# Optimization experiments

Hardware: AMD Instinct MI355X
Metric: run time of the kernel (lower is better)

The kernel has to match this reference:

```python
import jax, jax.numpy as jnp
import numpy as np

N_NODES = 100000
N_EDGES = 3200000
IN_DIM, BIG, HID = 4, 32, 2
EPS = 1e-5


def _lin_init(key, fan_in, fan_out):
    # torch nn.Linear default: U(-1/sqrt(fan_in), 1/sqrt(fan_in))
    kw, kb = jax.random.split(key)
    bound = 1.0 / np.sqrt(fan_in)
    w = jax.random.uniform(kw, (fan_in, fan_out), minval=-bound, maxval=bound, dtype=jnp.float32)
    b = jax.random.uniform(kb, (fan_out,), minval=-bound, maxval=bound, dtype=jnp.float32)
    return w, b


def setup_inputs() -> dict:
    key = jax.random.key(0)
    ks = jax.random.split(key, 9)
    x = jax.random.normal(ks[0], (N_NODES, IN_DIM), dtype=jnp.float32)
    edge_index = jax.random.randint(ks[1], (2, N_EDGES), 0, N_NODES, dtype=jnp.int32)
    bn_w = jnp.ones((IN_DIM,), jnp.float32)
    bn_b = jnp.zeros((IN_DIM,), jnp.float32)
    enc_w1, enc_b1 = _lin_init(ks[2], 2 * IN_DIM, BIG)
    enc_w2, enc_b2 = _lin_init(ks[3], BIG, BIG)
    enc_w3, enc_b3 = _lin_init(ks[4], BIG, HID)
    dec_w1, dec_b1 = _lin_init(ks[5], 2 * HID, BIG)
    dec_w2, dec_b2 = _lin_init(ks[6], BIG, BIG)
    dec_w3, dec_b3 = _lin_init(ks[7], BIG, IN_DIM)
    return dict(x=x, edge_index=edge_index, bn_w=bn_w, bn_b=bn_b,
                enc_w1=enc_w1, enc_b1=enc_b1, enc_w2=enc_w2, enc_b2=enc_b2,
                enc_w3=enc_w3, enc_b3=enc_b3,
                dec_w1=dec_w1, dec_b1=dec_b1, dec_w2=dec_w2, dec_b2=dec_b2,
                dec_w3=dec_w3, dec_b3=dec_b3)


def _edge_conv(x, src, dst, w1, b1, w2, b2, w3, b3, final_relu):
    # PyG EdgeConv: message = nn(cat([x_i, x_j - x_i])), mean-aggregated at target i (=dst)
    xi = x[dst]                     # [E, F] gather (target)
    xj = x[src]                     # [E, F] gather (source)
    h = jnp.concatenate([xi, xj - xi], axis=-1)  # [E, 2F]
    h = jax.nn.relu(h @ w1 + b1)
    h = jax.nn.relu(h @ w2 + b2)
    h = h @ w3 + b3
    if final_relu:
        h = jax.nn.relu(h)
    n = x.shape[0]
    agg = jax.ops.segment_sum(h, dst, num_segments=n)          # [N, out]
    cnt = jax.ops.segment_sum(jnp.ones((h.shape[0],), h.dtype), dst, num_segments=n)
    return agg / jnp.maximum(cnt, 1.0)[:, None]


def reference(x, edge_index, bn_w, bn_b,
              enc_w1, enc_b1, enc_w2, enc_b2, enc_w3, enc_b3,
              dec_w1, dec_b1, dec_w2, dec_b2, dec_w3, dec_b3):
    # BatchNorm1d (training mode: batch statistics, biased variance)
    mu = jnp.mean(x, axis=0)
    var = jnp.var(x, axis=0)
    h = (x - mu) * jax.lax.rsqrt(var + EPS) * bn_w + bn_b
    src, dst = edge_index[0], edge_index[1]
    h = _edge_conv(h, src, dst, enc_w1, enc_b1, enc_w2, enc_b2, enc_w3, enc_b3, final_relu=True)
    h = _edge_conv(h, src, dst, dec_w1, dec_b1, dec_w2, dec_b2, dec_w3, dec_b3, final_relu=False)
    return h
```

## Files before the change

### kernel.cpp

```cpp
#include <hip/hip_runtime.h>

#define N_NODES 100000
#define N_EDGES 3200000
#define EPS 1e-5f
#define NODE_BLOCKS 391
#define NB 782
#define BSTRIDE 4608
#define NSUB 9
#define S1_EPB 8192
#define S1_BLOCKS 391

typedef unsigned int uint;
typedef uint u32x4 __attribute__((ext_vector_type(4)));
typedef _Float16 f16x8 __attribute__((ext_vector_type(8)));
typedef float f32x16 __attribute__((ext_vector_type(16)));

static __device__ __forceinline__ f16x8 as_h8(u32x4 u) { return __builtin_bit_cast(f16x8, u); }
static __device__ __forceinline__ uint pkh(float a, float b) {
    return __builtin_bit_cast(uint, __builtin_amdgcn_cvt_pkrtz(a, b));
}
static __device__ __forceinline__ void swap32(uint& a, uint& b) {
    asm volatile("v_permlane32_swap_b32 %0, %1" : "+v"(a), "+v"(b));
}

#define OFF_STATS  0
#define OFF_BCNT   1024
#define OFF_INVCNT 5120
#define OFF_AGG1   405120
#define OFF_DECW   1205120
#define OFF_BUCKET 1214848
#define OFF_PENC   15629696
#define OFF_PCNT   22836608
#define OFF_PDEC   26440064
#define OFF_ENCW   26440064

__global__ __launch_bounds__(256) void k_bn_stats(const float* __restrict__ x,
                                                  double* __restrict__ stats) {
    int i = blockIdx.x * 256 + threadIdx.x;
    float4 v = make_float4(0.f, 0.f, 0.f, 0.f);
    if (i < N_NODES) v = ((const float4*)x)[i];
    double a[8];
    a[0] = v.x; a[1] = v.y; a[2] = v.z; a[3] = v.w;
    a[4] = (double)v.x * v.x; a[5] = (double)v.y * v.y;
    a[6] = (double)v.z * v.z; a[7] = (double)v.w * v.w;
    #pragma unroll
    for (int off = 32; off > 0; off >>= 1) {
        #pragma unroll
        for (int j = 0; j < 8; j++) a[j] += __shfl_down(a[j], off);
    }
    __shared__ double smem[4][8];
    int wave = threadIdx.x >> 6;
    int lane = threadIdx.x & 63;
    if (lane == 0) {
        #pragma unroll
        for (int j = 0; j < 8; j++) smem[wave][j] = a[j];
    }
    __syncthreads();
    if (threadIdx.x == 0) {
        #pragma unroll
        for (int j = 0; j < 8; j++) {
            double t = smem[0][j] + smem[1][j] + smem[2][j] + smem[3][j];
            atomicAdd(&stats[j], t);
        }
    }
}

static __device__ __forceinline__ void packhl(float v0, float v1, uint* ph, uint* pl) {
    _Float16 h0 = (_Float16)v0, h1 = (_Float16)v1;
    float r0 = v0 - (float)h0, r1 = v1 - (float)h1;
    _Float16 l0 = (_Float16)r0, l1 = (_Float16)r1;
    *ph = (uint)__builtin_bit_cast(unsigned short, h0) |
          ((uint)__builtin_bit_cast(unsigned short, h1) << 16);
    *pl = (uint)__builtin_bit_cast(unsigned short, l0) |
          ((uint)__builtin_bit_cast(unsigned short, l1) << 16);
}

__global__ __launch_bounds__(256) void k_prep(const float* __restrict__ ew1,
                                              const float* __restrict__ eb1,
                                              const float* __restrict__ ew2,
                                              const float* __restrict__ dw1,
                                              const float* __restrict__ db1,
                                              const float* __restrict__ dw2,
                                              uint* __restrict__ encw,
                                              uint* __restrict__ decw) {
    int t = threadIdx.x;
    int lane = t >> 2, d = t & 3, hi = lane >> 5, m = lane & 31;
    int k0 = 8 * hi + 2 * d;
    uint h, l;
    {
        float v0 = (k0 < 8) ? ew1[k0 * 32 + m] : (k0 == 8 ? eb1[m] : 0.f);
        float v1 = (k0 + 1 < 8) ? ew1[(k0 + 1) * 32 + m] : 0.f;
        packhl(v0, v1, &h, &l);
        encw[t] = h; encw[256 + t] = l;
    }
    #pragma unroll
    for (int kt = 0; kt < 2; kt++) {
        int k = 16 * kt + k0;
        packhl(ew2[k * 32 + m], ew2[(k + 1) * 32 + m], &h, &l);
        encw[512 + kt * 256 + t] = h; encw[1024 + kt * 256 + t] = l;
    }
    {
        float v0 = (k0 < 4) ? dw1[k0 * 32 + m] : (k0 == 4 ? db1[m] : 0.f);
        float v1 = (k0 + 1 < 4) ? dw1[(k0 + 1) * 32 + m] : 0.f;
        packhl(v0, v1, &h, &l);
        decw[t] = h; decw[256 + t] = l;
    }
    #pragma unroll
    for (int kt = 0; kt < 2; kt++) {
        int k = 16 * kt + k0;
        packhl(dw2[k * 32 + m], dw2[(k + 1) * 32 + m], &h, &l);
        decw[512 + kt * 256 + t] = h; decw[1024 + kt * 256 + t] = l;
    }
}

__global__ __launch_bounds__(256) void k_s1(const int* __restrict__ ei,
                                            int* __restrict__ bcnt,
                                            int* __restrict__ bucket_buf) {
    __shared__ int hist[NB];
    __shared__ int base[NB];
    __shared__ int run[NB];
    __shared__ int gbase[NB];
    __shared__ int entries[S1_EPB];
    __shared__ unsigned short bk16[S1_EPB];
    __shared__ int wsum[4];
    int tid = threadIdx.x;
    int e0 = blockIdx.x * S1_EPB;
    for (int i = tid; i < NB; i += 256) hist[i] = 0;
    __syncthreads();
    #pragma unroll
    for (int k = 0; k < 32; k++) {
        int e = e0 + k * 256 + tid;
        if (e < N_EDGES) atomicAdd(&hist[ei[N_EDGES + e] >> 7], 1);
    }
    __syncthreads();
    int t4 = tid * 4;
    int h0 = (t4 + 0 < NB) ? hist[t4 + 0] : 0;
    int h1 = (t4 + 1 < NB) ? hist[t4 + 1] : 0;
    int h2 = (t4 + 2 < NB) ? hist[t4 + 2] : 0;
    int h3 = (t4 + 3 < NB) ? hist[t4 + 3] : 0;
    int tsum = h0 + h1 + h2 + h3;
    int lane = tid & 63, wv = tid >> 6;
    int xs = tsum;
    #pragma unroll
    for (int off = 1; off < 64; off <<= 1) {
        int u = __shfl_up(xs, off);
        if (lane >= off) xs += u;
    }
    if (lane == 63) wsum[wv] = xs;
    __syncthreads();
    int wo = 0;
    #pragma unroll
    for (int w = 0; w < 4; w++) if (w < wv) wo += wsum[w];
    int texcl = wo + xs - tsum;
    if (t4 + 0 < NB) base[t4 + 0] = texcl;
    if (t4 + 1 < NB) base[t4 + 1] = texcl + h0;
    if (t4 + 2 < NB) base[t4 + 2] = texcl + h0 + h1;
    if (t4 + 3 < NB) base[t4 + 3] = texcl + h0 + h1 + h2;
    __syncthreads();
    for (int i = tid; i < NB; i += 256) {
        int h = hist[i];
        gbase[i] = i * BSTRIDE + (h ? atomicAdd(&bcnt[i], h) : 0);
        run[i] = base[i];
    }
    __syncthreads();
    #pragma unroll
    for (int k = 0; k < 32; k++) {
        int e = e0 + k * 256 + tid;
        if (e < N_EDGES) {
            int s = ei[e];
            int d = ei[N_EDGES + e];
            int b = d >> 7;
            int r = atomicAdd(&run[b], 1);
            entries[r] = s | ((d & 127) << 17);
            bk16[r] = (unsigned short)b;
        }
    }
    __syncthreads();
    int nloc = min(S1_EPB, N_EDGES - e0);
    for (int idx = tid; idx < nloc; idx += 256) {
        int b = bk16[idx];
        bucket_buf[gbase[b] + (idx - base[b])] = entries[idx];
    }
}

__global__ __launch_bounds__(256, 3) void k_enc_partial(const float* __restrict__ x,
                                                        const double* __restrict__ stats,
                                                        const float* __restrict__ bn_w,
                                                        const float* __restrict__ bn_b,
                                                        const int* __restrict__ bucket_buf,
                                                        const int* __restrict__ bcnt,
                                                        float2* __restrict__ penc,
                                                        int* __restrict__ pcnt,
                                                        const uint* __restrict__ encw,
                                                        const float* __restrict__ b2,
                                                        const float* __restrict__ w3,
                                                        const float* __restrict__ b3) {
    __shared__ float4 xhat[128];
    __shared__ float acc0[128], acc1[128];
    __shared__ int lc[128];
    __shared__ __align__(8) float w3s[64];
    int b = blockIdx.x, sub = blockIdx.y, tid = threadIdx.x;
    int lane = tid & 63, hi = lane >> 5, col = lane & 31, wv = tid >> 6;
    int cb = bcnt[b];
    int node0 = b << 7;

    const double inv_n = 1.0 / (double)N_NODES;
    float sc[4], sh[4];
    #pragma unroll
    for (int d = 0; d < 4; d++) {
        double m  = stats[d] * inv_n;
        double vr = stats[4 + d] * inv_n - m * m;
        float rs  = (float)(1.0 / sqrt(vr + (double)EPS));
        sc[d] = rs * bn_w[d];
        sh[d] = bn_b[d] - (float)m * sc[d];
    }

    if (tid < 128) {
        acc0[tid] = 0.f; acc1[tid] = 0.f; lc[tid] = 0;
        int n = node0 + tid;
        if (n < N_NODES) {
            float4 v = ((const float4*)x)[n];
            xhat[tid] = make_float4(fmaf(v.x, sc[0], sh[0]), fmaf(v.y, sc[1], sh[1]),
                                    fmaf(v.z, sc[2], sh[2]), fmaf(v.w, sc[3], sh[3]));
        }
    }
    if (tid < 64) w3s[tid] = w3[tid];
    __syncthreads();

    const u32x4* e4 = (const u32x4*)encw;
    u32x4 w1h = e4[lane],        w1l = e4[64 + lane];
    u32x4 w2h0 = e4[128 + lane], w2h1 = e4[192 + lane];
    u32x4 w2l0 = e4[256 + lane], w2l1 = e4[320 + lane];
    float b2v[16];
    #pragma unroll
    for (int r = 0; r < 16; r++) b2v[r] = b2[(r & 3) + 8 * (r >> 2) + 4 * hi];
    float b30 = b3[0], b31 = b3[1];

    u32x4 xf;
    xf.x = hi ? 0x00003C00u : 0u;
    xf.y = 0u; xf.z = 0u; xf.w = 0u;

    if (sub * 512 < cb) {
        #pragma unroll 1
        for (int t = 0; t < 4; t++) {
            int slot = sub * 512 + wv * 128 + t * 32 + col;
            bool valid = (hi == 0) && (slot < cb);
            int ia = 0;
            if (hi == 0) {
                int e = valid ? bucket_buf[b * BSTRIDE + slot] : 0;
                int s = e & 0x1FFFF;
                ia = (e >> 17) & 127;
                float4 xj = ((const float4*)x)[s];
                float4 xi = xhat[ia];
                float j0 = fmaf(xj.x, sc[0], sh[0]) - xi.x;
                float j1 = fmaf(xj.y, sc[1], sh[1]) - xi.y;
                float j2 = fmaf(xj.z, sc[2], sh[2]) - xi.z;
                float j3 = fmaf(xj.w, sc[3], sh[3]) - xi.w;
                xf.x = pkh(xi.x, xi.y);
                xf.y = pkh(xi.z, xi.w);
                xf.z = pkh(j0, j1);
                xf.w = pkh(j2, j3);
            }
            f32x16 c = {};
            c = __builtin_amdgcn_mfma_f32_32x32x16_f16(as_h8(w1h), as_h8(xf), c, 0, 0, 0);
            c = __builtin_amdgcn_mfma_f32_32x32x16_f16(as_h8(w1l), as_h8(xf), c, 0, 0, 0);
            #pragma unroll
            for (int r = 0; r < 16; r++) c[r] = fmaxf(c[r], 0.f);
            uint p0 = pkh(c[0], c[1]),   p1 = pkh(c[2], c[3]);
            uint q0 = pkh(c[4], c[5]),   q1 = pkh(c[6], c[7]);
            uint p2 = pkh(c[8], c[9]),   p3 = pkh(c[10], c[11]);
            uint q2 = pkh(c[12], c[13]), q3 = pkh(c[14], c[15]);
            swap32(p0, q0); swap32(p1, q1);
            swap32(p2, q2); swap32(p3, q3);
            u32x4 f0; f0.x = p0; f0.y = p1; f0.z = q0; f0.w = q1;
            u32x4 f1; f1.x = p2; f1.y = p3; f1.z = q2; f1.w = q3;
            f32x16 c2;
            #pragma unroll
            for (int r = 0; r < 16; r++) c2[r] = b2v[r];
            c2 = __builtin_amdgcn_mfma_f32_32x32x16_f16(as_h8(w2h0), as_h8(f0), c2, 0, 0, 0);
            c2 = __builtin_amdgcn_mfma_f32_32x32x16_f16(as_h8(w2h1), as_h8(f1), c2, 0, 0, 0);
            c2 = __builtin_amdgcn_mfma_f32_32x32x16_f16(as_h8(w2l0), as_h8(f0), c2, 0, 0, 0);
            c2 = __builtin_amdgcn_mfma_f32_32x32x16_f16(as_h8(w2l1), as_h8(f1), c2, 0, 0, 0);
            float o0 = 0.f, o1 = 0.f;
            #pragma unroll
            for (int r = 0; r < 16; r++) {
                float h2 = fmaxf(c2[r], 0.f);
                float2 w = *(const float2*)&w3s[2 * ((r & 3) + 8 * (r >> 2)) + 8 * hi];
                o0 = fmaf(h2, w.x, o0);
                o1 = fmaf(h2, w.y, o1);
            }
            o0 += __shfl_xor(o0, 32);
            o1 += __shfl_xor(o1, 32);
            if (valid) {
                o0 = fmaxf(o0 + b30, 0.f);
                o1 = fmaxf(o1 + b31, 0.f);
                atomicAdd(&acc0[ia], o0);
                atomicAdd(&acc1[ia], o1);
                atomicAdd(&lc[ia], 1);
            }
        }
    }
    __syncthreads();
    if (tid < 128) {
        int pb = b * NSUB + sub;
        penc[pb * 128 + tid] = make_float2(acc0[tid], acc1[tid]);
        pcnt[pb * 128 + tid] = lc[tid];
    }
}

__global__ __launch_bounds__(256) void k_reduce_enc_p(const float2* __restrict__ penc,
                                                      const int* __restrict__ pcnt,
                                                      float2* __restrict__ agg1,
                                                      float* __restrict__ invcnt) {
    int i = blockIdx.x * 256 + threadIdx.x;
    if (i >= N_NODES) return;
    int b = i >> 7, l = i & 127;
    float a0 = 0.f, a1 = 0.f;
    int c = 0;
    #pragma unroll
    for (int sub = 0; sub < NSUB; sub++) {
        int idx = (b * NSUB + sub) * 128 + l;
        float2 p = penc[idx];
        a0 += p.x; a1 += p.y;
        c += pcnt[idx];
    }
    float ic = 1.0f / (float)(c > 1 ? c : 1);
    invcnt[i] = ic;
    agg1[i] = make_float2(a0 * ic, a1 * ic);
}

__global__ __launch_bounds__(256, 3) void k_dec_partial(const float2* __restrict__ henc,
                                                        const int* __restrict__ bucket_buf,
                                                        const int* __restrict__ bcnt,
                                                        float4* __restrict__ pdec,
                                                        const uint* __restrict__ decw,
                                                        const float* __restrict__ b2,
                                                        const float* __restrict__ w3,
                                                        const float* __restrict__ b3) {
    __shared__ float2 hld[128];
    __shared__ float a0s[128], a1s[128], a2s[128], a3s[128];
    __shared__ __align__(16) float w3s[128];
    int b = blockIdx.x, sub = blockIdx.y, tid = threadIdx.x;
    int lane = tid & 63, hi = lane >> 5, col = lane & 31, wv = tid >> 6;
    int cb = bcnt[b];
    int node0 = b << 7;

    if (tid < 128) {
        a0s[tid] = 0.f; a1s[tid] = 0.f; a2s[tid] = 0.f; a3s[tid] = 0.f;
        int n = node0 + tid;
        if (n < N_NODES) hld[tid] = henc[n];
        w3s[tid] = w3[tid];
    }
    __syncthreads();

    const u32x4* d4 = (const u32x4*)decw;
    u32x4 v1h = d4[lane],        v1l = d4[64 + lane];
    u32x4 v2h0 = d4[128 + lane], v2h1 = d4[192 + lane];
    u32x4 v2l0 = d4[256 + lane], v2l1 = d4[320 + lane];
    float b2v[16];
    #pragma unroll
    for (int r = 0; r < 16; r++) b2v[r] = b2[(r & 3) + 8 * (r >> 2) + 4 * hi];
    float b3v[4] = {b3[0], b3[1], b3[2], b3[3]};

    u32x4 xf;
    xf.x = 0u; xf.y = 0u;
    xf.z = hi ? 0u : 0x00003C00u;
    xf.w = 0u;

    if (sub * 512 < cb) {
        #pragma unroll 1
        for (int t = 0; t < 4; t++) {
            int slot = sub * 512 + wv * 128 + t * 32 + col;
            bool valid = (hi == 0) && (slot < cb);
            int ia = 0;
            if (hi == 0) {
                int e = valid ? bucket_buf[b * BSTRIDE + slot] : 0;
                int s = e & 0x1FFFF;
                ia = (e >> 17) & 127;
                float2 hj = henc[s];
                float2 hi2 = hld[ia];
                xf.x = pkh(hi2.x, hi2.y);
                xf.y = pkh(hj.x - hi2.x, hj.y - hi2.y);
            }
            f32x16 c = {};
            c = __builtin_amdgcn_mfma_f32_32x32x16_f16(as_h8(v1h), as_h8(xf), c, 0, 0, 0);
            c = __builtin_amdgcn_mfma_f32_32x32x16_f16(as_h8(v1l), as_h8(xf), c, 0, 0, 0);
            #pragma unroll
            for (int r = 0; r < 16; r++) c[r] = fmaxf(c[r], 0.f);
            uint p0 = pkh(c[0], c[1]),   p1 = pkh(c[2], c[3]);
            uint q0 = pkh(c[4], c[5]),   q1 = pkh(c[6], c[7]);
            uint p2 = pkh(c[8], c[9]),   p3 = pkh(c[10], c[11]);
            uint q2 = pkh(c[12], c[13]), q3 = pkh(c[14], c[15]);
            swap32(p0, q0); swap32(p1, q1);
            swap32(p2, q2); swap32(p3, q3);
            u32x4 f0; f0.x = p0; f0.y = p1; f0.z = q0; f0.w = q1;
            u32x4 f1; f1.x = p2; f1.y = p3; f1.z = q2; f1.w = q3;
            f32x16 c2;
            #pragma unroll
            for (int r = 0; r < 16; r++) c2[r] = b2v[r];
            c2 = __builtin_amdgcn_mfma_f32_32x32x16_f16(as_h8(v2h0), as_h8(f0), c2, 0, 0, 0);
            c2 = __builtin_amdgcn_mfma_f32_32x32x16_f16(as_h8(v2h1), as_h8(f1), c2, 0, 0, 0);
            c2 = __builtin_amdgcn_mfma_f32_32x32x16_f16(as_h8(v2l0), as_h8(f0), c2, 0, 0, 0);
            c2 = __builtin_amdgcn_mfma_f32_32x32x16_f16(as_h8(v2l1), as_h8(f1), c2, 0, 0, 0);
            float o0 = 0.f, o1 = 0.f, o2 = 0.f, o3 = 0.f;
            #pragma unroll
            for (int r = 0; r < 16; r++) {
                float h2 = fmaxf(c2[r], 0.f);
                float4 w = *(const float4*)&w3s[4 * ((r & 3) + 8 * (r >> 2)) + 16 * hi];
                o0 = fmaf(h2, w.x, o0);
                o1 = fmaf(h2, w.y, o1);
                o2 = fmaf(h2, w.z, o2);
                o3 = fmaf(h2, w.w, o3);
            }
            o0 += __shfl_xor(o0, 32);
            o1 += __shfl_xor(o1, 32);
            o2 += __shfl_xor(o2, 32);
            o3 += __shfl_xor(o3, 32);
            if (valid) {
                atomicAdd(&a0s[ia], o0 + b3v[0]);
                atomicAdd(&a1s[ia], o1 + b3v[1]);
                atomicAdd(&a2s[ia], o2 + b3v[2]);
                atomicAdd(&a3s[ia], o3 + b3v[3]);
            }
        }
    }
    __syncthreads();
    if (tid < 128) {
        int pb = b * NSUB + sub;
        pdec[pb * 128 + tid] = make_float4(a0s[tid], a1s[tid], a2s[tid], a3s[tid]);
    }
}

__global__ __launch_bounds__(256) void k_reduce_dec_p(const float4* __restrict__ pdec,
                                                      const float* __restrict__ invcnt,
                                                      float4* __restrict__ out) {
    int i = blockIdx.x * 256 + threadIdx.x;
    if (i >= N_NODES) return;
    int b = i >> 7, l = i & 127;
    float a0 = 0.f, a1 = 0.f, a2 = 0.f, a3 = 0.f;
    #pragma unroll
    for (int sub = 0; sub < NSUB; sub++) {
        float4 p = pdec[(b * NSUB + sub) * 128 + l];
        a0 += p.x; a1 += p.y; a2 += p.z; a3 += p.w;
    }
    float ic = invcnt[i];
    out[i] = make_float4(a0 * ic, a1 * ic, a2 * ic, a3 * ic);
}

extern "C" void kernel_launch(void* const* d_in, const int* in_sizes, int n_in,
                              void* d_out, int out_size, void* d_ws, size_t ws_size,
                              hipStream_t stream) {
    const float* x    = (const float*)d_in[0];
    const int*   ei   = (const int*)d_in[1];
    const float* bn_w = (const float*)d_in[2];
    const float* bn_b = (const float*)d_in[3];
    const float* ew1  = (const float*)d_in[4];
    const float* eb1  = (const float*)d_in[5];
    const float* ew2  = (const float*)d_in[6];
    const float* eb2  = (const float*)d_in[7];
    const float* ew3  = (const float*)d_in[8];
    const float* eb3  = (const float*)d_in[9];
    const float* dw1  = (const float*)d_in[10];
    const float* db1  = (const float*)d_in[11];
    const float* dw2  = (const float*)d_in[12];
    const float* db2  = (const float*)d_in[13];
    const float* dw3  = (const float*)d_in[14];
    const float* db3  = (const float*)d_in[15];

    char* ws = (char*)d_ws;
    double* stats      = (double*)(ws + OFF_STATS);
    int*    bcnt       = (int*)(ws + OFF_BCNT);
    float*  invcnt     = (float*)(ws + OFF_INVCNT);
    float2* agg1       = (float2*)(ws + OFF_AGG1);
    uint*   decw       = (uint*)(ws + OFF_DECW);
    int*    bucket_buf = (int*)(ws + OFF_BUCKET);
    float2* penc       = (float2*)(ws + OFF_PENC);
    int*    pcnt       = (int*)(ws + OFF_PCNT);
    float4* pdec       = (float4*)(ws + OFF_PDEC);
    uint*   encw       = (uint*)(ws + OFF_ENCW);
    float4* out        = (float4*)d_out;

    hipMemsetAsync(ws, 0, 5120, stream);

    k_prep<<<1, 256, 0, stream>>>(ew1, eb1, ew2, dw1, db1, dw2, encw, decw);
    k_bn_stats<<<NODE_BLOCKS, 256, 0, stream>>>(x, stats);
    k_s1<<<S1_BLOCKS, 256, 0, stream>>>(ei, bcnt, bucket_buf);
    k_enc_partial<<<dim3(NB, NSUB), 256, 0, stream>>>(x, stats, bn_w, bn_b,
                                                      bucket_buf, bcnt, penc, pcnt,
                                                      encw, eb2, ew3, eb3);
    k_reduce_enc_p<<<NODE_BLOCKS, 256, 0, stream>>>(penc, pcnt, agg1, invcnt);
    k_dec_partial<<<dim3(NB, NSUB), 256, 0, stream>>>(agg1, bucket_buf, bcnt, pdec,
                                                      decw, db2, dw3, db3);
    k_reduce_dec_p<<<NODE_BLOCKS, 256, 0, stream>>>(pdec, invcnt, out);
}
```

Baseline: 330.8 us.

## Fold BatchNorm into weights, run layer 3 on MFMA, batch edge gathers

k_prep now runs after the stats kernel. It folds the BatchNorm scale into the first encoder weights and its shift into the first bias. It packs fp16 hi/lo splits so the hi and lo parts share one MFMA along the K dimension, and packs the third layer's weights and all biases for MFMA use. The encoder and decoder partial kernels now initialise accumulators from the biases and apply ReLU with packed fp16 max. They replace the scalar FMA loop and cross-half shuffles of the last layer with four MFMAs. Each thread loads its four edge entries with one int4 and issues all four gathers before computing. This removes per-block BN math, shared-memory weight staging and serial gather latency, at the cost of extra MFMAs on a mostly padded output tile and more register pressure.

After: 305.9 us. 7.5% less time.

```diff
diff --git a/kernel.cpp b/kernel.cpp
--- a/kernel.cpp
+++ b/kernel.cpp
@@ -13,6 +13,7 @@
 typedef unsigned int uint;
 typedef uint u32x4 __attribute__((ext_vector_type(4)));
 typedef _Float16 f16x8 __attribute__((ext_vector_type(8)));
+typedef _Float16 f16x2 __attribute__((ext_vector_type(2)));
 typedef float f32x16 __attribute__((ext_vector_type(16)));
 
 static __device__ __forceinline__ f16x8 as_h8(u32x4 u) { return __builtin_bit_cast(f16x8, u); }
@@ -21,6 +22,24 @@
 }
 static __device__ __forceinline__ void swap32(uint& a, uint& b) {
     asm volatile("v_permlane32_swap_b32 %0, %1" : "+v"(a), "+v"(b));
+}
+static __device__ __forceinline__ uint prelu(uint u, uint z) {
+    uint r;
+    asm("v_pk_max_f16 %0, %1, %2" : "=v"(r) : "v"(u), "v"(z));
+    return r;
+}
+
+#define MFMA(A, B, C) __builtin_amdgcn_mfma_f32_32x32x16_f16(as_h8(A), as_h8(B), (C), 0, 0, 0)
+
+static __device__ __forceinline__ void repack(const f32x16& c, u32x4& f0, u32x4& f1, uint z) {
+    uint p0 = prelu(pkh(c[0], c[1]), z),   p1 = prelu(pkh(c[2], c[3]), z);
+    uint q0 = prelu(pkh(c[4], c[5]), z),   q1 = prelu(pkh(c[6], c[7]), z);
+    uint p2 = prelu(pkh(c[8], c[9]), z),   p3 = prelu(pkh(c[10], c[11]), z);
+    uint q2 = prelu(pkh(c[12], c[13]), z), q3 = prelu(pkh(c[14], c[15]), z);
+    swap32(p0, q0); swap32(p1, q1);
+    swap32(p2, q2); swap32(p3, q3);
+    f0.x = p0; f0.y = p1; f0.z = q0; f0.w = q1;
+    f1.x = p2; f1.y = p3; f1.z = q2; f1.w = q3;
 }
 
 #define OFF_STATS  0
@@ -34,6 +53,7 @@
 #define OFF_PDEC   26440064
 #define OFF_ENCW   26440064
 
+
 __global__ __launch_bounds__(256) void k_bn_stats(const float* __restrict__ x,
                                                   double* __restrict__ stats) {
     int i = blockIdx.x * 256 + threadIdx.x;
@@ -65,51 +85,98 @@
     }
 }
 
-static __device__ __forceinline__ void packhl(float v0, float v1, uint* ph, uint* pl) {
-    _Float16 h0 = (_Float16)v0, h1 = (_Float16)v1;
-    float r0 = v0 - (float)h0, r1 = v1 - (float)h1;
-    _Float16 l0 = (_Float16)r0, l1 = (_Float16)r1;
-    *ph = (uint)__builtin_bit_cast(unsigned short, h0) |
-          ((uint)__builtin_bit_cast(unsigned short, h1) << 16);
-    *pl = (uint)__builtin_bit_cast(unsigned short, l0) |
-          ((uint)__builtin_bit_cast(unsigned short, l1) << 16);
-}
-
-__global__ __launch_bounds__(256) void k_prep(const float* __restrict__ ew1,
+static __device__ __forceinline__ uint pk_part(float a, float b, int part) {
+    _Float16 ah = (_Float16)a, bh = (_Float16)b;
+    if (part) {
+        a -= (float)ah; b -= (float)bh;
+        ah = (_Float16)a; bh = (_Float16)b;
+    }
+    return (uint)__builtin_bit_cast(unsigned short, ah) |
+           ((uint)__builtin_bit_cast(unsigned short, bh) << 16);
+}
+
+__global__ __launch_bounds__(256) void k_prep(const double* __restrict__ stats,
+                                              const float* __restrict__ bn_w,
+                                              const float* __restrict__ bn_b,
+                                              const float* __restrict__ ew1,
                                               const float* __restrict__ eb1,
                                               const float* __restrict__ ew2,
+                                              const float* __restrict__ eb2,
+                                              const float* __restrict__ ew3,
+                                              const float* __restrict__ eb3,
                                               const float* __restrict__ dw1,
                                               const float* __restrict__ db1,
                                               const float* __restrict__ dw2,
+                                              const float* __restrict__ db2,
+                                              const float* __restrict__ dw3,
+                                              const float* __restrict__ db3,
                                               uint* __restrict__ encw,
                                               uint* __restrict__ decw) {
     int t = threadIdx.x;
-    int lane = t >> 2, d = t & 3, hi = lane >> 5, m = lane & 31;
-    int k0 = 8 * hi + 2 * d;
-    uint h, l;
+    int lane = t >> 2, d = t & 3;
+    int hi = lane >> 5, m = lane & 31;
+
+    const double inv_n = 1.0 / (double)N_NODES;
+    float sc[4], sh[4];
+    #pragma unroll
+    for (int dd = 0; dd < 4; dd++) {
+        double mu = stats[dd] * inv_n;
+        double vr = stats[4 + dd] * inv_n - mu * mu;
+        float rs = (float)(1.0 / sqrt(vr + (double)EPS));
+        sc[dd] = rs * bn_w[dd];
+        sh[dd] = bn_b[dd] - (float)mu * sc[dd];
+    }
+
     {
-        float v0 = (k0 < 8) ? ew1[k0 * 32 + m] : (k0 == 8 ? eb1[m] : 0.f);
-        float v1 = (k0 + 1 < 8) ? ew1[(k0 + 1) * 32 + m] : 0.f;
-        packhl(v0, v1, &h, &l);
-        encw[t] = h; encw[256 + t] = l;
-    }
-    #pragma unroll
-    for (int kt = 0; kt < 2; kt++) {
-        int k = 16 * kt + k0;
-        packhl(ew2[k * 32 + m], ew2[(k + 1) * 32 + m], &h, &l);
-        encw[512 + kt * 256 + t] = h; encw[1024 + kt * 256 + t] = l;
+        int j = 2 * d;
+        float a = ew1[j * 32 + m] * sc[j & 3];
+        float bb = ew1[(j + 1) * 32 + m] * sc[(j + 1) & 3];
+        encw[t] = pk_part(a, bb, hi);
     }
     {
-        float v0 = (k0 < 4) ? dw1[k0 * 32 + m] : (k0 == 4 ? db1[m] : 0.f);
-        float v1 = (k0 + 1 < 4) ? dw1[(k0 + 1) * 32 + m] : 0.f;
-        packhl(v0, v1, &h, &l);
-        decw[t] = h; decw[256 + t] = l;
-    }
-    #pragma unroll
-    for (int kt = 0; kt < 2; kt++) {
-        int k = 16 * kt + k0;
-        packhl(dw2[k * 32 + m], dw2[(k + 1) * 32 + m], &h, &l);
-        decw[512 + kt * 256 + t] = h; decw[1024 + kt * 256 + t] = l;
+        int j = 2 * d;
+        float a = (j < 4) ? dw1[j * 32 + m] : 0.f;
+        float bb = (j + 1 < 4) ? dw1[(j + 1) * 32 + m] : 0.f;
+        decw[t] = pk_part(a, bb, hi);
+    }
+    #pragma unroll
+    for (int tile = 0; tile < 2; tile++) {
+        int k = 16 * tile + 8 * hi + 2 * d;
+        {
+            float a = ew2[k * 32 + m], bb = ew2[(k + 1) * 32 + m];
+            encw[256 + tile * 256 + t] = pk_part(a, bb, 0);
+            encw[768 + tile * 256 + t] = pk_part(a, bb, 1);
+        }
+        {
+            float a = dw2[k * 32 + m], bb = dw2[(k + 1) * 32 + m];
+            decw[256 + tile * 256 + t] = pk_part(a, bb, 0);
+            decw[768 + tile * 256 + t] = pk_part(a, bb, 1);
+        }
+        {
+            float a = (m < 2) ? ew3[k * 2 + m] : 0.f;
+            float bb = (m < 2) ? ew3[(k + 1) * 2 + m] : 0.f;
+            encw[1280 + tile * 256 + t] = pk_part(a, bb, 0);
+            encw[1792 + tile * 256 + t] = pk_part(a, bb, 1);
+        }
+        {
+            float a = (m < 4) ? dw3[k * 4 + m] : 0.f;
+            float bb = (m < 4) ? dw3[(k + 1) * 4 + m] : 0.f;
+            decw[1280 + tile * 256 + t] = pk_part(a, bb, 0);
+            decw[1792 + tile * 256 + t] = pk_part(a, bb, 1);
+        }
+    }
+    if (t < 32) {
+        int hh = t >> 4, r = t & 15;
+        int row = (r & 3) + 8 * (r >> 2) + 4 * hh;
+        float b1p = eb1[row];
+        #pragma unroll
+        for (int dd = 0; dd < 4; dd++) b1p += ew1[dd * 32 + row] * sh[dd];
+        ((float*)encw)[2304 + t] = b1p;
+        ((float*)encw)[2336 + t] = eb2[row];
+        ((float*)encw)[2368 + t] = (row < 2) ? eb3[row] : 0.f;
+        ((float*)decw)[2304 + t] = db1[row];
+        ((float*)decw)[2336 + t] = db2[row];
+        ((float*)decw)[2368 + t] = (row < 4) ? db3[row] : 0.f;
     }
 }
 
@@ -184,119 +251,92 @@
 }
 
 __global__ __launch_bounds__(256, 3) void k_enc_partial(const float* __restrict__ x,
-                                                        const double* __restrict__ stats,
-                                                        const float* __restrict__ bn_w,
-                                                        const float* __restrict__ bn_b,
                                                         const int* __restrict__ bucket_buf,
                                                         const int* __restrict__ bcnt,
                                                         float2* __restrict__ penc,
                                                         int* __restrict__ pcnt,
-                                                        const uint* __restrict__ encw,
-                                                        const float* __restrict__ b2,
-                                                        const float* __restrict__ w3,
-                                                        const float* __restrict__ b3) {
-    __shared__ float4 xhat[128];
+                                                        const uint* __restrict__ encw) {
+    __shared__ float4 xs[128];
     __shared__ float acc0[128], acc1[128];
     __shared__ int lc[128];
-    __shared__ __align__(8) float w3s[64];
     int b = blockIdx.x, sub = blockIdx.y, tid = threadIdx.x;
     int lane = tid & 63, hi = lane >> 5, col = lane & 31, wv = tid >> 6;
     int cb = bcnt[b];
     int node0 = b << 7;
 
-    const double inv_n = 1.0 / (double)N_NODES;
-    float sc[4], sh[4];
-    #pragma unroll
-    for (int d = 0; d < 4; d++) {
-        double m  = stats[d] * inv_n;
-        double vr = stats[4 + d] * inv_n - m * m;
-        float rs  = (float)(1.0 / sqrt(vr + (double)EPS));
-        sc[d] = rs * bn_w[d];
-        sh[d] = bn_b[d] - (float)m * sc[d];
-    }
-
     if (tid < 128) {
         acc0[tid] = 0.f; acc1[tid] = 0.f; lc[tid] = 0;
         int n = node0 + tid;
-        if (n < N_NODES) {
-            float4 v = ((const float4*)x)[n];
-            xhat[tid] = make_float4(fmaf(v.x, sc[0], sh[0]), fmaf(v.y, sc[1], sh[1]),
-                                    fmaf(v.z, sc[2], sh[2]), fmaf(v.w, sc[3], sh[3]));
-        }
-    }
-    if (tid < 64) w3s[tid] = w3[tid];
-    __syncthreads();
-
-    const u32x4* e4 = (const u32x4*)encw;
-    u32x4 w1h = e4[lane],        w1l = e4[64 + lane];
-    u32x4 w2h0 = e4[128 + lane], w2h1 = e4[192 + lane];
-    u32x4 w2l0 = e4[256 + lane], w2l1 = e4[320 + lane];
-    float b2v[16];
-    #pragma unroll
-    for (int r = 0; r < 16; r++) b2v[r] = b2[(r & 3) + 8 * (r >> 2) + 4 * hi];
-    float b30 = b3[0], b31 = b3[1];
-
-    u32x4 xf;
-    xf.x = hi ? 0x00003C00u : 0u;
-    xf.y = 0u; xf.z = 0u; xf.w = 0u;
+        if (n >= N_NODES) n = 0;
+        xs[tid] = ((const float4*)x)[n];
+    }
+    __syncthreads();
+
+    const u32x4* W4 = (const u32x4*)encw;
+    u32x4 w1   = W4[lane];
+    u32x4 w2h0 = W4[64 + lane],  w2h1 = W4[128 + lane];
+    u32x4 w2l0 = W4[192 + lane], w2l1 = W4[256 + lane];
+    u32x4 u3h0 = W4[320 + lane], u3h1 = W4[384 + lane];
+    u32x4 u3l0 = W4[448 + lane], u3l1 = W4[512 + lane];
+    const float* tf = (const float*)encw;
+    f32x16 b1f, b2f, b3f;
+    {
+        const float4* p1 = (const float4*)(tf + 2304 + hi * 16);
+        const float4* p2 = (const float4*)(tf + 2336 + hi * 16);
+        const float4* p3 = (const float4*)(tf + 2368 + hi * 16);
+        #pragma unroll
+        for (int q = 0; q < 4; q++) {
+            float4 a = p1[q], c = p2[q], e = p3[q];
+            b1f[4 * q] = a.x; b1f[4 * q + 1] = a.y; b1f[4 * q + 2] = a.z; b1f[4 * q + 3] = a.w;
+            b2f[4 * q] = c.x; b2f[4 * q + 1] = c.y; b2f[4 * q + 2] = c.z; b2f[4 * q + 3] = c.w;
+            b3f[4 * q] = e.x; b3f[4 * q + 1] = e.y; b3f[4 * q + 2] = e.z; b3f[4 * q + 3] = e.w;
+        }
+    }
+    uint z = 0;
 
     if (sub * 512 < cb) {
-        #pragma unroll 1
+        int sbase = sub * 512 + col * 16 + wv * 4;
+        int4 q = *(const int4*)&bucket_buf[b * BSTRIDE + sbase];
+        int ents[4] = {q.x, q.y, q.z, q.w};
+        int ss[4], ia[4];
+        #pragma unroll
         for (int t = 0; t < 4; t++) {
-            int slot = sub * 512 + wv * 128 + t * 32 + col;
-            bool valid = (hi == 0) && (slot < cb);
-            int ia = 0;
-            if (hi == 0) {
-                int e = valid ? bucket_buf[b * BSTRIDE + slot] : 0;
-                int s = e & 0x1FFFF;
-                ia = (e >> 17) & 127;
-                float4 xj = ((const float4*)x)[s];
-                float4 xi = xhat[ia];
-                float j0 = fmaf(xj.x, sc[0], sh[0]) - xi.x;
-                float j1 = fmaf(xj.y, sc[1], sh[1]) - xi.y;
-                float j2 = fmaf(xj.z, sc[2], sh[2]) - xi.z;
-                float j3 = fmaf(xj.w, sc[3], sh[3]) - xi.w;
-                xf.x = pkh(xi.x, xi.y);
-                xf.y = pkh(xi.z, xi.w);
-                xf.z = pkh(j0, j1);
-                xf.w = pkh(j2, j3);
-            }
-            f32x16 c = {};
-            c = __builtin_amdgcn_mfma_f32_32x32x16_f16(as_h8(w1h), as_h8(xf), c, 0, 0, 0);
-            c = __builtin_amdgcn_mfma_f32_32x32x16_f16(as_h8(w1l), as_h8(xf), c, 0, 0, 0);
-            #pragma unroll
-            for (int r = 0; r < 16; r++) c[r] = fmaxf(c[r], 0.f);
-            uint p0 = pkh(c[0], c[1]),   p1 = pkh(c[2], c[3]);
-            uint q0 = pkh(c[4], c[5]),   q1 = pkh(c[6], c[7]);
-            uint p2 = pkh(c[8], c[9]),   p3 = pkh(c[10], c[11]);
-            uint q2 = pkh(c[12], c[13]), q3 = pkh(c[14], c[15]);
-            swap32(p0, q0); swap32(p1, q1);
-            swap32(p2, q2); swap32(p3, q3);
-            u32x4 f0; f0.x = p0; f0.y = p1; f0.z = q0; f0.w = q1;
-            u32x4 f1; f1.x = p2; f1.y = p3; f1.z = q2; f1.w = q3;
-            f32x16 c2;
-            #pragma unroll
-            for (int r = 0; r < 16; r++) c2[r] = b2v[r];
-            c2 = __builtin_amdgcn_mfma_f32_32x32x16_f16(as_h8(w2h0), as_h8(f0), c2, 0, 0, 0);
-            c2 = __builtin_amdgcn_mfma_f32_32x32x16_f16(as_h8(w2h1), as_h8(f1), c2, 0, 0, 0);
-            c2 = __builtin_amdgcn_mfma_f32_32x32x16_f16(as_h8(w2l0), as_h8(f0), c2, 0, 0, 0);
-            c2 = __builtin_amdgcn_mfma_f32_32x32x16_f16(as_h8(w2l1), as_h8(f1), c2, 0, 0, 0);
-            float o0 = 0.f, o1 = 0.f;
-            #pragma unroll
-            for (int r = 0; r < 16; r++) {
-                float h2 = fmaxf(c2[r], 0.f);
-                float2 w = *(const float2*)&w3s[2 * ((r & 3) + 8 * (r >> 2)) + 8 * hi];
-                o0 = fmaf(h2, w.x, o0);
-                o1 = fmaf(h2, w.y, o1);
-            }
-            o0 += __shfl_xor(o0, 32);
-            o1 += __shfl_xor(o1, 32);
-            if (valid) {
-                o0 = fmaxf(o0 + b30, 0.f);
-                o1 = fmaxf(o1 + b31, 0.f);
-                atomicAdd(&acc0[ia], o0);
-                atomicAdd(&acc1[ia], o1);
-                atomicAdd(&lc[ia], 1);
+            int s = ents[t] & 0x1FFFF;
+            if (s >= N_NODES) s = 0;
+            ss[t] = s;
+            ia[t] = (ents[t] >> 17) & 127;
+        }
+        float4 xj[4];
+        #pragma unroll
+        for (int t = 0; t < 4; t++) xj[t] = ((const float4*)x)[ss[t]];
+
+        #pragma unroll
+        for (int t = 0; t < 4; t++) {
+            float4 xi = xs[ia[t]];
+            u32x4 xf;
+            xf.x = pkh(xi.x, xi.y);
+            xf.y = pkh(xi.z, xi.w);
+            xf.z = pkh(xj[t].x - xi.x, xj[t].y - xi.y);
+            xf.w = pkh(xj[t].z - xi.z, xj[t].w - xi.w);
+            f32x16 c = MFMA(w1, xf, b1f);
+            u32x4 f0, f1;
+            repack(c, f0, f1, z);
+            f32x16 c2 = MFMA(w2h0, f0, b2f);
+            c2 = MFMA(w2h1, f1, c2);
+            c2 = MFMA(w2l0, f0, c2);
+            c2 = MFMA(w2l1, f1, c2);
+            u32x4 e0, e1;
+            repack(c2, e0, e1, z);
+            f32x16 c3 = MFMA(u3h0, e0, b3f);
+            c3 = MFMA(u3h1, e1, c3);
+            c3 = MFMA(u3l0, e0, c3);
+            c3 = MFMA(u3l1, e1, c3);
+            if (hi == 0 && (sbase + t) < cb) {
+                float o0 = fmaxf(c3[0], 0.f);
+                float o1 = fmaxf(c3[1], 0.f);
+                atomicAdd(&acc0[ia[t]], o0);
+                atomicAdd(&acc1[ia[t]], o1);
+                atomicAdd(&lc[ia[t]], 1);
             }
         }
     }
@@ -333,13 +373,9 @@
                                                         const int* __restrict__ bucket_buf,
                                                         const int* __restrict__ bcnt,
                                                         float4* __restrict__ pdec,
-                                                        const uint* __restrict__ decw,
-                                                        const float* __restrict__ b2,
-                                                        const float* __restrict__ w3,
-                                                        const float* __restrict__ b3) {
+                                                        const uint* __restrict__ decw) {
     __shared__ float2 hld[128];
     __shared__ float a0s[128], a1s[128], a2s[128], a3s[128];
-    __shared__ __align__(16) float w3s[128];
     int b = blockIdx.x, sub = blockIdx.y, tid = threadIdx.x;
     int lane = tid & 63, hi = lane >> 5, col = lane & 31, wv = tid >> 6;
     int cb = bcnt[b];
@@ -348,79 +384,75 @@
     if (tid < 128) {
         a0s[tid] = 0.f; a1s[tid] = 0.f; a2s[tid] = 0.f; a3s[tid] = 0.f;
         int n = node0 + tid;
-        if (n < N_NODES) hld[tid] = henc[n];
-        w3s[tid] = w3[tid];
-    }
-    __syncthreads();
-
-    const u32x4* d4 = (const u32x4*)decw;
-    u32x4 v1h = d4[lane],        v1l = d4[64 + lane];
-    u32x4 v2h0 = d4[128 + lane], v2h1 = d4[192 + lane];
-    u32x4 v2l0 = d4[256 + lane], v2l1 = d4[320 + lane];
-    float b2v[16];
-    #pragma unroll
-    for (int r = 0; r < 16; r++) b2v[r] = b2[(r & 3) + 8 * (r >> 2) + 4 * hi];
-    float b3v[4] = {b3[0], b3[1], b3[2], b3[3]};
-
-    u32x4 xf;
-    xf.x = 0u; xf.y = 0u;
-    xf.z = hi ? 0u : 0x00003C00u;
-    xf.w = 0u;
+        if (n >= N_NODES) n = 0;
+        hld[tid] = henc[n];
+    }
+    __syncthreads();
+
+    const u32x4* W4 = (const u32x4*)decw;
+    u32x4 v1   = W4[lane];
+    u32x4 v2h0 = W4[64 + lane],  v2h1 = W4[128 + lane];
+    u32x4 v2l0 = W4[192 + lane], v2l1 = W4[256 + lane];
+    u32x4 u3h0 = W4[320 + lane], u3h1 = W4[384 + lane];
+    u32x4 u3l0 = W4[448 + lane], u3l1 = W4[512 + lane];
+    const float* tf = (const float*)decw;
+    f32x16 b1f, b2f, b3f;
+    {
+        const float4* p1 = (const float4*)(tf + 2304 + hi * 16);
+        const float4* p2 = (const float4*)(tf + 2336 + hi * 16);
+        const float4* p3 = (const float4*)(tf + 2368 + hi * 16);
+        #pragma unroll
+        for (int q = 0; q < 4; q++) {
+            float4 a = p1[q], c = p2[q], e = p3[q];
+            b1f[4 * q] = a.x; b1f[4 * q + 1] = a.y; b1f[4 * q + 2] = a.z; b1f[4 * q + 3] = a.w;
+            b2f[4 * q] = c.x; b2f[4 * q + 1] = c.y; b2f[4 * q + 2] = c.z; b2f[4 * q + 3] = c.w;
+            b3f[4 * q] = e.x; b3f[4 * q + 1] = e.y; b3f[4 * q + 2] = e.z; b3f[4 * q + 3] = e.w;
+        }
+    }
+    uint z = 0;
 
     if (sub * 512 < cb) {
-        #pragma unroll 1
+        int sbase = sub * 512 + col * 16 + wv * 4;
+        int4 q = *(const int4*)&bucket_buf[b * BSTRIDE + sbase];
+        int ents[4] = {q.x, q.y, q.z, q.w};
+        int ss[4], ia[4];
+        #pragma unroll
         for (int t = 0; t < 4; t++) {
-            int slot = sub * 512 + wv * 128 + t * 32 + col;
-            bool valid = (hi == 0) && (slot < cb);
-            int ia = 0;
-            if (hi == 0) {
-                int e = valid ? bucket_buf[b * BSTRIDE + slot] : 0;
-                int s = e & 0x1FFFF;
-                ia = (e >> 17) & 127;
-                float2 hj = henc[s];
-                float2 hi2 = hld[ia];
-                xf.x = pkh(hi2.x, hi2.y);
-                xf.y = pkh(hj.x - hi2.x, hj.y - hi2.y);
-            }
-            f32x16 c = {};
-            c = __builtin_amdgcn_mfma_f32_32x32x16_f16(as_h8(v1h), as_h8(xf), c, 0, 0, 0);
-            c = __builtin_amdgcn_mfma_f32_32x32x16_f16(as_h8(v1l), as_h8(xf), c, 0, 0, 0);
-            #pragma unroll
-            for (int r = 0; r < 16; r++) c[r] = fmaxf(c[r], 0.f);
-            uint p0 = pkh(c[0], c[1]),   p1 = pkh(c[2], c[3]);
-            uint q0 = pkh(c[4], c[5]),   q1 = pkh(c[6], c[7]);
-            uint p2 = pkh(c[8], c[9]),   p3 = pkh(c[10], c[11]);
-            uint q2 = pkh(c[12], c[13]), q3 = pkh(c[14], c[15]);
-            swap32(p0, q0); swap32(p1, q1);
-            swap32(p2, q2); swap32(p3, q3);
-            u32x4 f0; f0.x = p0; f0.y = p1; f0.z = q0; f0.w = q1;
-            u32x4 f1; f1.x = p2; f1.y = p3; f1.z = q2; f1.w = q3;
-            f32x16 c2;
-            #pragma unroll
-            for (int r = 0; r < 16; r++) c2[r] = b2v[r];
-            c2 = __builtin_amdgcn_mfma_f32_32x32x16_f16(as_h8(v2h0), as_h8(f0), c2, 0, 0, 0);
-            c2 = __builtin_amdgcn_mfma_f32_32x32x16_f16(as_h8(v2h1), as_h8(f1), c2, 0, 0, 0);
-            c2 = __builtin_amdgcn_mfma_f32_32x32x16_f16(as_h8(v2l0), as_h8(f0), c2, 0, 0, 0);
-            c2 = __builtin_amdgcn_mfma_f32_32x32x16_f16(as_h8(v2l1), as_h8(f1), c2, 0, 0, 0);
-            float o0 = 0.f, o1 = 0.f, o2 = 0.f, o3 = 0.f;
-            #pragma unroll
-            for (int r = 0; r < 16; r++) {
-                float h2 = fmaxf(c2[r], 0.f);
-                float4 w = *(const float4*)&w3s[4 * ((r & 3) + 8 * (r >> 2)) + 16 * hi];
-                o0 = fmaf(h2, w.x, o0);
-                o1 = fmaf(h2, w.y, o1);
-                o2 = fmaf(h2, w.z, o2);
-                o3 = fmaf(h2, w.w, o3);
-            }
-            o0 += __shfl_xor(o0, 32);
-            o1 += __shfl_xor(o1, 32);
-            o2 += __shfl_xor(o2, 32);
-            o3 += __shfl_xor(o3, 32);
-            if (valid) {
-                atomicAdd(&a0s[ia], o0 + b3v[0]);
-                atomicAdd(&a1s[ia], o1 + b3v[1]);
-                atomicAdd(&a2s[ia], o2 + b3v[2]);
-                atomicAdd(&a3s[ia], o3 + b3v[3]);
+            int s = ents[t] & 0x1FFFF;
+            if (s >= N_NODES) s = 0;
+            ss[t] = s;
+            ia[t] = (ents[t] >> 17) & 127;
+        }
+        float2 hj[4], hiv[4];
+        #pragma unroll
+        for (int t = 0; t < 4; t++) hj[t] = henc[ss[t]];
+        #pragma unroll
+        for (int t = 0; t < 4; t++) hiv[t] = hld[ia[t]];
+
+        #pragma unroll
+        for (int t = 0; t < 4; t++) {
+            u32x4 xf;
+            xf.x = pkh(hiv[t].x, hiv[t].y);
+            xf.y = pkh(hj[t].x - hiv[t].x, hj[t].y - hiv[t].y);
+            xf.z = 0u; xf.w = 0u;
+            f32x16 c = MFMA(v1, xf, b1f);
+            u32x4 f0, f1;
+            repack(c, f0, f1, z);
+            f32x16 c2 = MFMA(v2h0, f0, b2f);
+            c2 = MFMA(v2h1, f1, c2);
+            c2 = MFMA(v2l0, f0, c2);
+            c2 = MFMA(v2l1, f1, c2);
+            u32x4 e0, e1;
+            repack(c2, e0, e1, z);
+            f32x16 c3 = MFMA(u3h0, e0, b3f);
+            c3 = MFMA(u3h1, e1, c3);
+            c3 = MFMA(u3l0, e0, c3);
+            c3 = MFMA(u3l1, e1, c3);
+            if (hi == 0 && (sbase + t) < cb) {
+                atomicAdd(&a0s[ia[t]], c3[0]);
+                atomicAdd(&a1s[ia[t]], c3[1]);
+                atomicAdd(&a2s[ia[t]], c3[2]);
+                atomicAdd(&a3s[ia[t]], c3[3]);
             }
         }
     }
@@ -482,14 +514,13 @@
 
     hipMemsetAsync(ws, 0, 5120, stream);
 
-    k_prep<<<1, 256, 0, stream>>>(ew1, eb1, ew2, dw1, db1, dw2, encw, decw);
     k_bn_stats<<<NODE_BLOCKS, 256, 0, stream>>>(x, stats);
+    k_prep<<<1, 256, 0, stream>>>(stats, bn_w, bn_b, ew1, eb1, ew2, eb2, ew3, eb3,
+                                  dw1, db1, dw2, db2, dw3, db3, encw, decw);
     k_s1<<<S1_BLOCKS, 256, 0, stream>>>(ei, bcnt, bucket_buf);
-    k_enc_partial<<<dim3(NB, NSUB), 256, 0, stream>>>(x, stats, bn_w, bn_b,
-                                                      bucket_buf, bcnt, penc, pcnt,
-                                                      encw, eb2, ew3, eb3);
+    k_enc_partial<<<dim3(NB, NSUB), 256, 0, stream>>>(x, bucket_buf, bcnt,
+                                                      penc, pcnt, encw);
     k_reduce_enc_p<<<NODE_BLOCKS, 256, 0, stream>>>(penc, pcnt, agg1, invcnt);
-    k_dec_partial<<<dim3(NB, NSUB), 256, 0, stream>>>(agg1, bucket_buf, bcnt, pdec,
-                                                      decw, db2, dw3, db3);
+    k_dec_partial<<<dim3(NB, NSUB), 256, 0, stream>>>(agg1, bucket_buf, bcnt, pdec, decw);
     k_reduce_dec_p<<<NODE_BLOCKS, 256, 0, stream>>>(pdec, invcnt, out);
 }
```
